# Kernel tuning notes

Hardware: AMD Instinct MI355X
Metric: run time of the kernel (lower is better)

The kernel has to match this reference:

```python
import jax, jax.numpy as jnp
import numpy as np

H = 8  # number of heads


def setup_inputs() -> dict:
    key = jax.random.key(0)
    ks = jax.random.split(key, 7)
    B, L, D = 4, 2048, 512
    dh = D // H
    s = 1.0 / np.sqrt(D).astype(np.float32)
    return {
        "q": jax.random.normal(ks[0], (B, L, D), jnp.float32),
        "k": jax.random.normal(ks[1], (B, L, D), jnp.float32),
        "v": jax.random.normal(ks[2], (B, L, D), jnp.float32),
        "Wq": jax.random.normal(ks[3], (D, D), jnp.float32) * s,
        "Wk": jax.random.normal(ks[4], (D, D), jnp.float32) * s,
        "Wv": jax.random.normal(ks[5], (D, D), jnp.float32) * s,
        "E": jax.random.normal(ks[6], (L, dh), jnp.float32) * s,
    }


def _skew(QE):
    # QE: [B, H, L, L] -> pad one column on the left, reshape to [B,H,L+1,L],
    # drop the first row: the classic Music Transformer skewing trick.
    B, h, L, M = QE.shape
    padded = jnp.pad(QE, ((0, 0), (0, 0), (0, 0), (1, 0)))
    return padded.reshape(B, h, M + 1, L)[:, :, 1:, :]


def reference(q, k, v, Wq, Wk, Wv, E):
    B, L, D = q.shape
    dh = D // H

    def heads(x, W):
        return jnp.einsum('bld,de->ble', x, W).reshape(B, L, H, dh).transpose(0, 2, 1, 3)

    qh = heads(q, Wq)  # [B,H,L,dh]
    kh = heads(k, Wk)
    vh = heads(v, Wv)

    QE = jnp.einsum('bhld,md->bhlm', qh, E)      # [B,H,L,L]
    Srel = _skew(QE)                             # [B,H,L,L]
    QKt = jnp.einsum('bhld,bhmd->bhlm', qh, kh)  # [B,H,L,L]

    # NOTE: original divides AFTER softmax (faithful to source).
    attn = jax.nn.softmax(QKt + Srel, axis=-1) / float(np.sqrt(dh))
    out = jnp.einsum('bhlm,bhmd->bhld', attn, vh)
    return out.transpose(0, 2, 1, 3).reshape(B, L, D)
```

## Files before the change

kernel.cpp:

```cpp
#include <hip/hip_runtime.h>
#include <hip/hip_bf16.h>
#include <math.h>

typedef _Float16 f16;
typedef __attribute__((ext_vector_type(8))) _Float16 f16x8;
typedef __attribute__((ext_vector_type(4))) _Float16 f16x4;
typedef __attribute__((ext_vector_type(4))) float f32x4;

namespace {
constexpr int B = 4, L = 2048, D = 512, NH = 8, DH = 64;
}

__device__ __forceinline__ float dpp_xor1(float x) {
    return __int_as_float(__builtin_amdgcn_update_dpp(0, __float_as_int(x), 0xB1, 0xF, 0xF, true));
}
__device__ __forceinline__ float dpp_xor2(float x) {
    return __int_as_float(__builtin_amdgcn_update_dpp(0, __float_as_int(x), 0x4E, 0xF, 0xF, true));
}

__global__ __launch_bounds__(256)
void ecast_kernel(const float* __restrict__ E, f16* __restrict__ Ef) {
    int i4 = (blockIdx.x * 256 + threadIdx.x) * 4;
    float4 x = *(const float4*)(E + i4);
    *(f16x4*)(Ef + i4) = (f16x4){(f16)x.x, (f16)x.y, (f16)x.z, (f16)x.w};
}

__global__ __launch_bounds__(256)
void xcast_kernel(const float* __restrict__ q, const float* __restrict__ k,
                  const float* __restrict__ v, f16* __restrict__ Xf) {
    const int sel = blockIdx.y;
    const float* X = (sel == 0) ? q : (sel == 1) ? k : v;
    const size_t i4 = ((size_t)blockIdx.x * 256 + threadIdx.x) * 4;
    float4 x = *(const float4*)(X + i4);
    *(f16x4*)(Xf + (size_t)sel * ((size_t)B * L * D) + i4) =
        (f16x4){(f16)x.x, (f16)x.y, (f16)x.z, (f16)x.w};
}

__global__ __launch_bounds__(256)
void wtrans_kernel(const float* __restrict__ Wq, const float* __restrict__ Wk,
                   const float* __restrict__ Wv, f16* __restrict__ Wt) {
    __shared__ f16 Ws[64 * 65];
    const int sel = blockIdx.z;
    const float* W = (sel == 0) ? Wq : (sel == 1) ? Wk : Wv;
    f16* Wo = Wt + (size_t)sel * D * D;
    const int k0 = blockIdx.x * 64, n0 = blockIdx.y * 64;
    const int t = threadIdx.x;
#pragma unroll
    for (int i = 0; i < 16; ++i) {
        int idx = 256 * i + t;
        int r = idx >> 6, c = idx & 63;
        Ws[r * 65 + c] = (f16)W[(size_t)(k0 + r) * D + n0 + c];
    }
    __syncthreads();
    const int c = t >> 2, kseg = t & 3;
    f16x8 r0, r1;
#pragma unroll
    for (int j = 0; j < 8; ++j) r0[j] = Ws[(kseg * 16 + j) * 65 + c];
#pragma unroll
    for (int j = 0; j < 8; ++j) r1[j] = Ws[(kseg * 16 + 8 + j) * 65 + c];
    f16* o = Wo + (size_t)(n0 + c) * D + k0 + kseg * 16;
    *(f16x8*)o = r0;
    *(f16x8*)(o + 8) = r1;
}

__global__ __launch_bounds__(256, 4)
void proj_gemm(const f16* __restrict__ Xf, const f16* __restrict__ Wt,
               f16* __restrict__ Qf, f16* __restrict__ Kf, f16* __restrict__ Vtf) {
    __shared__ f16 As[128 * 72];
    __shared__ f16 Bs[64 * 72];
    const int flat = blockIdx.x;
    const int wg = (flat & 7) * 192 + (flat >> 3);
    const int by = wg % 24, bx = wg / 24;
    const int sel = by >> 3, h = by & 7;
    const int m0 = bx * 128;
    const f16* X = Xf + (size_t)sel * ((size_t)B * L * D);
    const f16* Bt = Wt + (size_t)sel * D * D + (size_t)h * 64 * D;
    const int t = threadIdx.x, wid = t >> 6, lane = t & 63;
    const int quad = lane >> 4, col = lane & 15;
    const int mw = wid * 32;

    f32x4 acc[2][4];
#pragma unroll
    for (int i = 0; i < 2; ++i)
#pragma unroll
        for (int j = 0; j < 4; ++j) acc[i][j] = (f32x4){0.f, 0.f, 0.f, 0.f};

    f16x8 xa[4];
    f16x8 breg[2];
    auto loadG = [&](int k0) {
#pragma unroll
        for (int i = 0; i < 4; ++i) {
            int idx = 256 * i + t;
            int r = idx >> 3, ch = idx & 7;
            xa[i] = *(const f16x8*)(X + (size_t)(m0 + r) * D + k0 + ch * 8);
        }
#pragma unroll
        for (int i = 0; i < 2; ++i) {
            int idx = 256 * i + t;
            int r = idx >> 3, ch = idx & 7;
            breg[i] = *(const f16x8*)(Bt + (size_t)r * D + k0 + ch * 8);
        }
    };
    auto storeL = [&]() {
#pragma unroll
        for (int i = 0; i < 4; ++i) {
            int idx = 256 * i + t;
            int r = idx >> 3, ch = idx & 7;
            *(f16x8*)(As + r * 72 + ch * 8) = xa[i];
        }
#pragma unroll
        for (int i = 0; i < 2; ++i) {
            int idx = 256 * i + t;
            int r = idx >> 3, ch = idx & 7;
            *(f16x8*)(Bs + r * 72 + ch * 8) = breg[i];
        }
    };

    loadG(0);
    for (int k0 = 0; k0 < D; k0 += 64) {
        __syncthreads();
        storeL();
        __syncthreads();
        if (k0 + 64 < D) loadG(k0 + 64);
#pragma unroll
        for (int ks = 0; ks < 2; ++ks) {
            f16x8 af[2], bf[4];
#pragma unroll
            for (int mt = 0; mt < 2; ++mt)
                af[mt] = *(const f16x8*)(As + (mw + mt * 16 + col) * 72 + quad * 8 + ks * 32);
#pragma unroll
            for (int nt = 0; nt < 4; ++nt)
                bf[nt] = *(const f16x8*)(Bs + (nt * 16 + col) * 72 + quad * 8 + ks * 32);
#pragma unroll
            for (int mt = 0; mt < 2; ++mt)
#pragma unroll
                for (int nt = 0; nt < 4; ++nt)
                    acc[mt][nt] = __builtin_amdgcn_mfma_f32_16x16x32_f16(af[mt], bf[nt], acc[mt][nt], 0, 0, 0);
        }
    }

    if (sel < 2) {
        f16* Y = (sel == 0) ? Qf : Kf;
#pragma unroll
        for (int mt = 0; mt < 2; ++mt)
#pragma unroll
            for (int nt = 0; nt < 4; ++nt)
#pragma unroll
                for (int reg = 0; reg < 4; ++reg) {
                    int m = m0 + mw + mt * 16 + quad * 4 + reg;
                    int bb = m >> 11, l = m & 2047, d = nt * 16 + col;
                    Y[((size_t)(bb * NH + h) * L + l) * DH + d] = (f16)acc[mt][nt][reg];
                }
    } else {
        __syncthreads();
        f16* Cs = As;
#pragma unroll
        for (int mt = 0; mt < 2; ++mt)
#pragma unroll
            for (int nt = 0; nt < 4; ++nt)
#pragma unroll
                for (int reg = 0; reg < 4; ++reg) {
                    int d = nt * 16 + col;
                    int lc = mw + mt * 16 + quad * 4 + reg;
                    Cs[d * 136 + lc] = (f16)acc[mt][nt][reg];
                }
        __syncthreads();
        const int dd = t >> 2, seg = t & 3;
        const int bb = m0 >> 11, l0 = m0 & 2047;
        f16* Yv = Vtf + ((size_t)(bb * NH + h) * DH + dd) * L + l0 + seg * 32;
#pragma unroll
        for (int j = 0; j < 4; ++j)
            *(f16x8*)(Yv + j * 8) = *(const f16x8*)(Cs + dd * 136 + seg * 32 + j * 8);
    }
}

__global__ __launch_bounds__(256, 4)
void attn_kernel(const f16* __restrict__ Qf, const f16* __restrict__ Kf,
                 const f16* __restrict__ Vtf, const f16* __restrict__ Ef,
                 float* __restrict__ out) {
    __shared__ f16 KfS[64 * 72];
    __shared__ f16 VfS[64 * 72];
    __shared__ f16 Pbuf[4][16 * 72];

    const int t = threadIdx.x, wid = t >> 6, lane = t & 63;
    const int quad = lane >> 4, col = lane & 15;
    const int l0w = blockIdx.x * 64 + wid * 16;
    const int h = blockIdx.y, bb = blockIdx.z;
    const size_t head = (size_t)(bb * NH + h) * (size_t)(L * DH);
    const f16* qf = Qf + head;
    const f16* kf = Kf + head;
    const f16* vt = Vtf + head;
    f16* Pw = Pbuf[wid];

    const f16x8 ones8 = {(f16)1.f, (f16)1.f, (f16)1.f, (f16)1.f,
                         (f16)1.f, (f16)1.f, (f16)1.f, (f16)1.f};

    f16x8 qF[2], qS[2];
    {
        const int m = l0w + col;
        const int mS = min(m + 1, L - 1);
#pragma unroll
        for (int ks = 0; ks < 2; ++ks) {
            const int off = quad * 8 + ks * 32;
            qF[ks] = *(const f16x8*)(qf + (size_t)m * DH + off);
            qS[ks] = *(const f16x8*)(qf + (size_t)mS * DH + off);
        }
    }

    f16x8 kreg[2], vreg[2];
    auto loadKV = [&](int c0) {
#pragma unroll
        for (int i = 0; i < 2; ++i) {
            int idx = 256 * i + t;
            int r = idx >> 3, ch = idx & 7;
            kreg[i] = *(const f16x8*)(kf + (size_t)(c0 + r) * DH + ch * 8);
            vreg[i] = *(const f16x8*)(vt + (size_t)r * L + c0 + ch * 8);
        }
    };

    f32x4 O[4];
#pragma unroll
    for (int i = 0; i < 4; ++i) O[i] = (f32x4){0.f, 0.f, 0.f, 0.f};
    f32x4 sacc = (f32x4){0.f, 0.f, 0.f, 0.f};
    float mrow[4] = {-1e30f, -1e30f, -1e30f, -1e30f};

    loadKV(0);
    for (int c0 = 0; c0 < L; c0 += 64) {
        __syncthreads();
#pragma unroll
        for (int i = 0; i < 2; ++i) {
            int idx = 256 * i + t;
            int r = idx >> 3, ch = idx & 7;
            *(f16x8*)(KfS + r * 72 + ch * 8) = kreg[i];
            *(f16x8*)(VfS + r * 72 + ch * 8) = vreg[i];
        }
        __syncthreads();
        if (c0 + 64 < L) loadKV(c0 + 64);

        const int d0 = c0 - l0w;

        f32x4 S[4];
        __builtin_amdgcn_s_setprio(1);
#pragma unroll
        for (int ns = 0; ns < 4; ++ns) {
            S[ns] = (f32x4){0.f, 0.f, 0.f, 0.f};
#pragma unroll
            for (int ks = 0; ks < 2; ++ks) {
                f16x8 bh = *(const f16x8*)(KfS + (ns * 16 + col) * 72 + quad * 8 + ks * 32);
                S[ns] = __builtin_amdgcn_mfma_f32_16x16x32_f16(qF[ks], bh, S[ns], 0, 0, 0);
            }
        }
        __builtin_amdgcn_s_setprio(0);

        const bool doA = (d0 <= 15);
        const bool doB = (d0 >= -61);
#pragma unroll 1
        for (int pass = 0; pass < 2; ++pass) {
            if ((pass == 0 && !doA) || (pass == 1 && !doB)) continue;
            const int jbase = (pass == 0) ? (d0 + L - 16) : (d0 - 17);
            f32x4 G[5];
#pragma unroll
            for (int g = 0; g < 5; ++g) {
                int er = min(max(jbase + g * 16 + col, 0), L - 1);
                G[g] = (f32x4){0.f, 0.f, 0.f, 0.f};
                const size_t eb = (size_t)er * DH + quad * 8;
#pragma unroll
                for (int ks = 0; ks < 2; ++ks) {
                    f16x8 e8 = *(const f16x8*)(Ef + eb + ks * 32);
                    G[g] = __builtin_amdgcn_mfma_f32_16x16x32_f16(
                               (pass == 0) ? qF[ks] : qS[ks], e8, G[g], 0, 0, 0);
                }
            }
#pragma unroll
            for (int reg = 0; reg < 4; ++reg) {
                const int r  = quad * 4 + reg;
                const int jj = col - r + 15;
                const int src = quad * 16 + (jj & 15);
#pragma unroll
                for (int ns = 0; ns < 4; ++ns) {
                    float v0 = __shfl(G[ns][reg], src, 64);
                    float v1 = __shfl(G[ns + 1][reg], src, 64);
                    float val = (jj < 16) ? v0 : v1;
                    const int rel = d0 + ns * 16 + col - r;
                    const bool use = (pass == 0) ? (rel <= 0) : (rel >= 2);
                    if (use) S[ns][reg] += val;
                }
            }
        }

#pragma unroll
        for (int reg = 0; reg < 4; ++reg) {
            float tm = fmaxf(fmaxf(S[0][reg], S[1][reg]), fmaxf(S[2][reg], S[3][reg]));
            tm = fmaxf(tm, dpp_xor1(tm));
            tm = fmaxf(tm, dpp_xor2(tm));
            tm = fmaxf(tm, __shfl_xor(tm, 4, 16));
            tm = fmaxf(tm, __shfl_xor(tm, 8, 16));
            const float mnew  = fmaxf(mrow[reg], tm);
            const float alpha = __expf(mrow[reg] - mnew);
            mrow[reg] = mnew;
            sacc[reg] *= alpha;
            const int r = quad * 4 + reg;
#pragma unroll
            for (int ns = 0; ns < 4; ++ns) {
                float p = __expf(S[ns][reg] - mnew);
                O[ns][reg] *= alpha;
                Pw[r * 72 + ns * 16 + col] = (f16)p;
            }
        }

        f16x8 pA[2];
        pA[0] = *(const f16x8*)(Pw + col * 72 + quad * 8);
        pA[1] = *(const f16x8*)(Pw + col * 72 + 32 + quad * 8);
        __builtin_amdgcn_s_setprio(1);
        sacc = __builtin_amdgcn_mfma_f32_16x16x32_f16(pA[0], ones8, sacc, 0, 0, 0);
        sacc = __builtin_amdgcn_mfma_f32_16x16x32_f16(pA[1], ones8, sacc, 0, 0, 0);
#pragma unroll
        for (int ns = 0; ns < 4; ++ns) {
#pragma unroll
            for (int ks = 0; ks < 2; ++ks) {
                f16x8 v8 = *(const f16x8*)(VfS + (ns * 16 + col) * 72 + quad * 8 + ks * 32);
                O[ns] = __builtin_amdgcn_mfma_f32_16x16x32_f16(pA[ks], v8, O[ns], 0, 0, 0);
            }
        }
        __builtin_amdgcn_s_setprio(0);
    }

#pragma unroll
    for (int reg = 0; reg < 4; ++reg) {
        const int l = l0w + quad * 4 + reg;
        const float inv = 1.0f / (sacc[reg] * 8.0f);
        float* o = out + ((size_t)bb * L + l) * D + h * DH;
#pragma unroll
        for (int ns = 0; ns < 4; ++ns)
            o[ns * 16 + col] = O[ns][reg] * inv;
    }
}

extern "C" void kernel_launch(void* const* d_in, const int* in_sizes, int n_in,
                              void* d_out, int out_size, void* d_ws, size_t ws_size,
                              hipStream_t stream) {
    const float* q  = (const float*)d_in[0];
    const float* k  = (const float*)d_in[1];
    const float* v  = (const float*)d_in[2];
    const float* Wq = (const float*)d_in[3];
    const float* Wk = (const float*)d_in[4];
    const float* Wv = (const float*)d_in[5];
    const float* E  = (const float*)d_in[6];
    float* out = (float*)d_out;

    const size_t plane = (size_t)B * NH * L * DH;
    f16* Qf  = (f16*)d_ws;
    f16* Kfp = Qf + plane;
    f16* Vtf = Kfp + plane;
    f16* Wt  = Vtf + plane;
    f16* Ef  = Wt + (size_t)3 * D * D;
    f16* Xf  = Ef + (size_t)L * DH;

    ecast_kernel<<<L * DH / 1024, 256, 0, stream>>>(E, Ef);
    xcast_kernel<<<dim3((unsigned)(plane / 1024), 3), 256, 0, stream>>>(q, k, v, Xf);
    wtrans_kernel<<<dim3(8, 8, 3), 256, 0, stream>>>(Wq, Wk, Wv, Wt);
    proj_gemm<<<dim3(1536), 256, 0, stream>>>(Xf, Wt, Qf, Kfp, Vtf);
    attn_kernel<<<dim3(L / 64, NH, B), 256, 0, stream>>>(Qf, Kfp, Vtf, Ef, out);
}
```

Baseline: 324.4 us.

## Enlarge projection GEMM tile, prefetch E rows, and streamline relative-position skew

The projection GEMM tile grows from 128 to 256 rows per block, giving each warp a 64x64 output and halving the grid. Occupancy drops from 4 to 3 blocks. In attention, E fragments for the first pass are loaded before the QK MFMAs so their latency overlaps. The skew step now has unmasked fast paths for tiles that lie entirely in one pass, and uses a single shuffle per element instead of two. Other changes: row-max reduction uses DPP rotates instead of shuffles, P-buffer writes use an XOR swizzle against bank conflicts, and the attention grid is remapped so blocks interleave across XCDs. The cost is more registers and lower occupancy in both kernels.

```diff
diff --git a/kernel.cpp b/kernel.cpp
--- a/kernel.cpp
+++ b/kernel.cpp
@@ -16,6 +16,12 @@
 }
 __device__ __forceinline__ float dpp_xor2(float x) {
     return __int_as_float(__builtin_amdgcn_update_dpp(0, __float_as_int(x), 0x4E, 0xF, 0xF, true));
+}
+__device__ __forceinline__ float dpp_ror4(float x) {
+    return __int_as_float(__builtin_amdgcn_update_dpp(0, __float_as_int(x), 0x124, 0xF, 0xF, true));
+}
+__device__ __forceinline__ float dpp_ror8(float x) {
+    return __int_as_float(__builtin_amdgcn_update_dpp(0, __float_as_int(x), 0x128, 0xF, 0xF, true));
 }
 
 __global__ __launch_bounds__(256)
@@ -63,33 +69,33 @@
     *(f16x8*)(o + 8) = r1;
 }
 
-__global__ __launch_bounds__(256, 4)
+__global__ __launch_bounds__(256, 3)
 void proj_gemm(const f16* __restrict__ Xf, const f16* __restrict__ Wt,
                f16* __restrict__ Qf, f16* __restrict__ Kf, f16* __restrict__ Vtf) {
-    __shared__ f16 As[128 * 72];
+    __shared__ f16 As[256 * 72];
     __shared__ f16 Bs[64 * 72];
     const int flat = blockIdx.x;
-    const int wg = (flat & 7) * 192 + (flat >> 3);
+    const int wg = (flat & 7) * 96 + (flat >> 3);
     const int by = wg % 24, bx = wg / 24;
     const int sel = by >> 3, h = by & 7;
-    const int m0 = bx * 128;
+    const int m0 = bx * 256;
     const f16* X = Xf + (size_t)sel * ((size_t)B * L * D);
     const f16* Bt = Wt + (size_t)sel * D * D + (size_t)h * 64 * D;
     const int t = threadIdx.x, wid = t >> 6, lane = t & 63;
     const int quad = lane >> 4, col = lane & 15;
-    const int mw = wid * 32;
-
-    f32x4 acc[2][4];
-#pragma unroll
-    for (int i = 0; i < 2; ++i)
+    const int mw = wid * 64;
+
+    f32x4 acc[4][4];
+#pragma unroll
+    for (int i = 0; i < 4; ++i)
 #pragma unroll
         for (int j = 0; j < 4; ++j) acc[i][j] = (f32x4){0.f, 0.f, 0.f, 0.f};
 
-    f16x8 xa[4];
+    f16x8 xa[8];
     f16x8 breg[2];
     auto loadG = [&](int k0) {
 #pragma unroll
-        for (int i = 0; i < 4; ++i) {
+        for (int i = 0; i < 8; ++i) {
             int idx = 256 * i + t;
             int r = idx >> 3, ch = idx & 7;
             xa[i] = *(const f16x8*)(X + (size_t)(m0 + r) * D + k0 + ch * 8);
@@ -103,7 +109,7 @@
     };
     auto storeL = [&]() {
 #pragma unroll
-        for (int i = 0; i < 4; ++i) {
+        for (int i = 0; i < 8; ++i) {
             int idx = 256 * i + t;
             int r = idx >> 3, ch = idx & 7;
             *(f16x8*)(As + r * 72 + ch * 8) = xa[i];
@@ -124,15 +130,15 @@
         if (k0 + 64 < D) loadG(k0 + 64);
 #pragma unroll
         for (int ks = 0; ks < 2; ++ks) {
-            f16x8 af[2], bf[4];
-#pragma unroll
-            for (int mt = 0; mt < 2; ++mt)
+            f16x8 af[4], bf[4];
+#pragma unroll
+            for (int mt = 0; mt < 4; ++mt)
                 af[mt] = *(const f16x8*)(As + (mw + mt * 16 + col) * 72 + quad * 8 + ks * 32);
 #pragma unroll
             for (int nt = 0; nt < 4; ++nt)
                 bf[nt] = *(const f16x8*)(Bs + (nt * 16 + col) * 72 + quad * 8 + ks * 32);
 #pragma unroll
-            for (int mt = 0; mt < 2; ++mt)
+            for (int mt = 0; mt < 4; ++mt)
 #pragma unroll
                 for (int nt = 0; nt < 4; ++nt)
                     acc[mt][nt] = __builtin_amdgcn_mfma_f32_16x16x32_f16(af[mt], bf[nt], acc[mt][nt], 0, 0, 0);
@@ -142,7 +148,7 @@
     if (sel < 2) {
         f16* Y = (sel == 0) ? Qf : Kf;
 #pragma unroll
-        for (int mt = 0; mt < 2; ++mt)
+        for (int mt = 0; mt < 4; ++mt)
 #pragma unroll
             for (int nt = 0; nt < 4; ++nt)
 #pragma unroll
@@ -155,22 +161,22 @@
         __syncthreads();
         f16* Cs = As;
 #pragma unroll
-        for (int mt = 0; mt < 2; ++mt)
+        for (int mt = 0; mt < 4; ++mt)
 #pragma unroll
             for (int nt = 0; nt < 4; ++nt)
 #pragma unroll
                 for (int reg = 0; reg < 4; ++reg) {
                     int d = nt * 16 + col;
                     int lc = mw + mt * 16 + quad * 4 + reg;
-                    Cs[d * 136 + lc] = (f16)acc[mt][nt][reg];
+                    Cs[d * 264 + lc] = (f16)acc[mt][nt][reg];
                 }
         __syncthreads();
         const int dd = t >> 2, seg = t & 3;
         const int bb = m0 >> 11, l0 = m0 & 2047;
-        f16* Yv = Vtf + ((size_t)(bb * NH + h) * DH + dd) * L + l0 + seg * 32;
-#pragma unroll
-        for (int j = 0; j < 4; ++j)
-            *(f16x8*)(Yv + j * 8) = *(const f16x8*)(Cs + dd * 136 + seg * 32 + j * 8);
+        f16* Yv = Vtf + ((size_t)(bb * NH + h) * DH + dd) * L + l0 + seg * 64;
+#pragma unroll
+        for (int j = 0; j < 8; ++j)
+            *(f16x8*)(Yv + j * 8) = *(const f16x8*)(Cs + dd * 264 + seg * 64 + j * 8);
     }
 }
 
@@ -184,8 +190,11 @@
 
     const int t = threadIdx.x, wid = t >> 6, lane = t & 63;
     const int quad = lane >> 4, col = lane & 15;
-    const int l0w = blockIdx.x * 64 + wid * 16;
-    const int h = blockIdx.y, bb = blockIdx.z;
+    const int flat = blockIdx.x;
+    const int wg = (flat & 7) * 128 + (flat >> 3);
+    const int xq = wg & 31, yz = wg >> 5;
+    const int h = yz & 7, bb = yz >> 3;
+    const int l0w = xq * 64 + wid * 16;
     const size_t head = (size_t)(bb * NH + h) * (size_t)(L * DH);
     const f16* qf = Qf + head;
     const f16* kf = Kf + head;
@@ -239,6 +248,17 @@
 
         const int d0 = c0 - l0w;
 
+        const int pass0 = (d0 <= 15) ? 0 : 1;
+        const int jb0 = (pass0 == 0) ? (d0 + L - 16) : (d0 - 17);
+        f16x8 ea[5][2];
+#pragma unroll
+        for (int g = 0; g < 5; ++g) {
+            int er = min(max(jb0 + g * 16 + col, 0), L - 1);
+            const f16* ep = Ef + (size_t)er * DH + quad * 8;
+            ea[g][0] = *(const f16x8*)(ep);
+            ea[g][1] = *(const f16x8*)(ep + 32);
+        }
+
         f32x4 S[4];
         __builtin_amdgcn_s_setprio(1);
 #pragma unroll
@@ -252,21 +272,21 @@
         }
         __builtin_amdgcn_s_setprio(0);
 
-        const bool doA = (d0 <= 15);
-        const bool doB = (d0 >= -61);
-#pragma unroll 1
-        for (int pass = 0; pass < 2; ++pass) {
-            if ((pass == 0 && !doA) || (pass == 1 && !doB)) continue;
+        auto srel = [&](int pass, bool pre, bool masked) {
             const int jbase = (pass == 0) ? (d0 + L - 16) : (d0 - 17);
             f32x4 G[5];
 #pragma unroll
             for (int g = 0; g < 5; ++g) {
-                int er = min(max(jbase + g * 16 + col, 0), L - 1);
                 G[g] = (f32x4){0.f, 0.f, 0.f, 0.f};
-                const size_t eb = (size_t)er * DH + quad * 8;
 #pragma unroll
                 for (int ks = 0; ks < 2; ++ks) {
-                    f16x8 e8 = *(const f16x8*)(Ef + eb + ks * 32);
+                    f16x8 e8;
+                    if (pre) {
+                        e8 = ea[g][ks];
+                    } else {
+                        int er = min(max(jbase + g * 16 + col, 0), L - 1);
+                        e8 = *(const f16x8*)(Ef + (size_t)er * DH + quad * 8 + ks * 32);
+                    }
                     G[g] = __builtin_amdgcn_mfma_f32_16x16x32_f16(
                                (pass == 0) ? qF[ks] : qS[ks], e8, G[g], 0, 0, 0);
                 }
@@ -276,16 +296,28 @@
                 const int r  = quad * 4 + reg;
                 const int jj = col - r + 15;
                 const int src = quad * 16 + (jj & 15);
+                const bool hs = (col >= 15 - r);
 #pragma unroll
                 for (int ns = 0; ns < 4; ++ns) {
-                    float v0 = __shfl(G[ns][reg], src, 64);
-                    float v1 = __shfl(G[ns + 1][reg], src, 64);
-                    float val = (jj < 16) ? v0 : v1;
-                    const int rel = d0 + ns * 16 + col - r;
-                    const bool use = (pass == 0) ? (rel <= 0) : (rel >= 2);
-                    if (use) S[ns][reg] += val;
+                    float H = hs ? G[ns][reg] : G[ns + 1][reg];
+                    float val = __shfl(H, src, 64);
+                    if (masked) {
+                        const int rel = d0 + ns * 16 + col - r;
+                        const bool use = (pass == 0) ? (rel <= 0) : (rel >= 2);
+                        if (use) S[ns][reg] += val;
+                    } else {
+                        S[ns][reg] += val;
+                    }
                 }
             }
+        };
+        if (d0 < -48) {
+            srel(0, true, false);
+        } else if (d0 > 16) {
+            srel(1, true, false);
+        } else {
+            if (d0 <= 15) srel(0, true, true);
+            if (d0 >= -61) srel(1, pass0 == 1, true);
         }
 
 #pragma unroll
@@ -293,24 +325,26 @@
             float tm = fmaxf(fmaxf(S[0][reg], S[1][reg]), fmaxf(S[2][reg], S[3][reg]));
             tm = fmaxf(tm, dpp_xor1(tm));
             tm = fmaxf(tm, dpp_xor2(tm));
-            tm = fmaxf(tm, __shfl_xor(tm, 4, 16));
-            tm = fmaxf(tm, __shfl_xor(tm, 8, 16));
+            tm = fmaxf(tm, dpp_ror4(tm));
+            tm = fmaxf(tm, dpp_ror8(tm));
             const float mnew  = fmaxf(mrow[reg], tm);
             const float alpha = __expf(mrow[reg] - mnew);
             mrow[reg] = mnew;
             sacc[reg] *= alpha;
             const int r = quad * 4 + reg;
+            const int sw = (r & 8) << 1;
 #pragma unroll
             for (int ns = 0; ns < 4; ++ns) {
                 float p = __expf(S[ns][reg] - mnew);
                 O[ns][reg] *= alpha;
-                Pw[r * 72 + ns * 16 + col] = (f16)p;
-            }
-        }
-
+                Pw[r * 72 + ((ns * 16 + col) ^ sw)] = (f16)p;
+            }
+        }
+
+        const int rsw = (col & 8) << 1;
         f16x8 pA[2];
-        pA[0] = *(const f16x8*)(Pw + col * 72 + quad * 8);
-        pA[1] = *(const f16x8*)(Pw + col * 72 + 32 + quad * 8);
+        pA[0] = *(const f16x8*)(Pw + col * 72 + ((quad * 8) ^ rsw));
+        pA[1] = *(const f16x8*)(Pw + col * 72 + ((quad * 8 + 32) ^ rsw));
         __builtin_amdgcn_s_setprio(1);
         sacc = __builtin_amdgcn_mfma_f32_16x16x32_f16(pA[0], ones8, sacc, 0, 0, 0);
         sacc = __builtin_amdgcn_mfma_f32_16x16x32_f16(pA[1], ones8, sacc, 0, 0, 0);
@@ -359,6 +393,6 @@
     ecast_kernel<<<L * DH / 1024, 256, 0, stream>>>(E, Ef);
     xcast_kernel<<<dim3((unsigned)(plane / 1024), 3), 256, 0, stream>>>(q, k, v, Xf);
     wtrans_kernel<<<dim3(8, 8, 3), 256, 0, stream>>>(Wq, Wk, Wv, Wt);
-    proj_gemm<<<dim3(1536), 256, 0, stream>>>(Xf, Wt, Qf, Kfp, Vtf);
-    attn_kernel<<<dim3(L / 64, NH, B), 256, 0, stream>>>(Qf, Kfp, Vtf, Ef, out);
-}
+    proj_gemm<<<dim3(768), 256, 0, stream>>>(Xf, Wt, Qf, Kfp, Vtf);
+    attn_kernel<<<dim3(1024), 256, 0, stream>>>(Qf, Kfp, Vtf, Ef, out);
+}
```

After: 511.3 us. +57.6%, slower.
